# Performance work log

Measured on AMD Instinct MI355X. Metric: run time of the kernel, lower is better.

Reference implementation:

```python
import jax, jax.numpy as jnp
import numpy as np

B, S, D = 2, 2048, 768
E, L = 4, 2
H = 4 * D  # dim_mlp = dim * mlp_ratio
EPS = 1e-6


def setup_inputs() -> dict:
    key = jax.random.key(0)
    ks = jax.random.split(key, 4)
    x = jax.random.normal(ks[0], (B, S, D), dtype=jnp.float32)
    expert_idx = jax.random.randint(ks[1], (B, S), 0, E, dtype=jnp.int32)
    # Linear weights: normal(std=0.02), biases zero (per init_weights).
    W1 = 0.02 * jax.random.normal(ks[2], (L, E, D, H), dtype=jnp.float32)
    b1 = jnp.zeros((L, E, H), dtype=jnp.float32)
    W2 = 0.02 * jax.random.normal(ks[3], (L, E, H, D), dtype=jnp.float32)
    b2 = jnp.zeros((L, E, D), dtype=jnp.float32)
    # LayerNorm: weight=1, bias=0 (per init_weights).
    ln_g = jnp.ones((L, D), dtype=jnp.float32)
    ln_b = jnp.zeros((L, D), dtype=jnp.float32)
    return {"x": x, "expert_idx": expert_idx, "W1": W1, "b1": b1,
            "W2": W2, "b2": b2, "ln_g": ln_g, "ln_b": ln_b}


def _layernorm(x, g, b):
    mu = jnp.mean(x, axis=-1, keepdims=True)
    var = jnp.mean(jnp.square(x - mu), axis=-1, keepdims=True)
    return (x - mu) * jax.lax.rsqrt(var + EPS) * g + b


def reference(x, expert_idx, W1, b1, W2, b2, ln_g, ln_b):
    # Eval mode: Dropout and DropPath are identity.
    idx = expert_idx[:, :, None, None]  # [B,S,1,1] for gather over expert axis
    for i in range(L):
        h = _layernorm(x, ln_g[i], ln_b[i])                       # [B,S,D]
        # All experts' FFNs computed densely (as in the torch module).
        a = jnp.einsum('bsd,edh->bseh', h, W1[i]) + b1[i]         # [B,S,E,H]
        a = jax.nn.gelu(a, approximate=False)                     # exact GELU (nn.GELU)
        y = jnp.einsum('bseh,ehd->bsed', a, W2[i]) + b2[i]        # [B,S,E,D] == feat_all
        # Per-token gather of the selected expert's slice.
        sel = jnp.take_along_axis(y, idx, axis=2)[:, :, 0, :]     # [B,S,D]
        x = x + sel
    return x
```

## Files before the change

### kernel.cpp

```cpp
#include <hip/hip_runtime.h>
#include <hip/hip_bf16.h>

#define T_TOK 4096
#define DD 768
#define HH 3072
#define EE 4
#define LL 2
#define NELT (T_TOK * DD)

typedef __attribute__((ext_vector_type(8))) short short8;
typedef __attribute__((ext_vector_type(4))) float f32x4;

__device__ __forceinline__ float bf2f(ushort u) { return __uint_as_float(((unsigned)u) << 16); }
__device__ __forceinline__ ushort f2bf(float f) {
  unsigned x = __float_as_uint(f);
  return (ushort)((x + 0x7fffu + ((x >> 16) & 1u)) >> 16);
}

__device__ __forceinline__ void gl2lds16(const void* g, void* l) {
  __builtin_amdgcn_global_load_lds((const __attribute__((address_space(1))) void*)g,
                                   (__attribute__((address_space(3))) void*)l, 16, 0, 0);
}

__global__ __launch_bounds__(256) void prep_kernel(const int* __restrict__ eidx,
                                                   int* __restrict__ inv,
                                                   int* __restrict__ meta) {
  __shared__ int cnt[EE], cur[EE], offs[EE];
  int t = threadIdx.x;
  if (t < EE) { cnt[t] = 0; cur[t] = 0; }
  __syncthreads();
  for (int i = t; i < T_TOK; i += 256) atomicAdd(&cnt[eidx[i]], 1);
  __syncthreads();
  if (t == 0) {
    int off = 0, nt = 0;
    for (int e = 0; e < EE; e++) {
      meta[e] = off; offs[e] = off;
      int c = cnt[e];
      int n = (c + 127) >> 7;
      for (int k = 0; k < n; k++) { meta[8 + nt] = e; meta[96 + nt] = k << 7; nt++; }
      off += c;
    }
    meta[4] = off;
    meta[5] = nt;
  }
  __syncthreads();
  for (int i = t; i < T_TOK; i += 256) {
    int e = eidx[i];
    inv[i] = offs[e] + atomicAdd(&cur[e], 1);
  }
}

template <bool HASY, bool WRITEX>
__global__ __launch_bounds__(256) void ln_kernel(const float* __restrict__ x,
                                                 const float* __restrict__ y,
                                                 const float* __restrict__ g,
                                                 const float* __restrict__ b,
                                                 const int* __restrict__ inv,
                                                 ushort* __restrict__ h,
                                                 float* __restrict__ xf) {
  int wid = blockIdx.x * 4 + (threadIdx.x >> 6);
  int lane = threadIdx.x & 63;
  int pos = inv[wid];
  const float* xr = x + (size_t)wid * DD;
  const float* y0 = y + (size_t)pos * DD;
  const float* y1 = y0 + NELT;
  float v[12], s = 0.f, ss = 0.f;
#pragma unroll
  for (int i = 0; i < 12; i++) {
    int c = lane + i * 64;
    float vv = xr[c];
    if (HASY) vv += y0[c] + y1[c];
    if (WRITEX) xf[(size_t)wid * DD + c] = vv;
    v[i] = vv;
    s += vv; ss += vv * vv;
  }
#pragma unroll
  for (int o = 32; o; o >>= 1) { s += __shfl_xor(s, o, 64); ss += __shfl_xor(ss, o, 64); }
  float mu = s * (1.f / DD);
  float var = ss * (1.f / DD) - mu * mu;
  float rs = rsqrtf(var + 1e-6f);
  ushort* hr = h + (size_t)pos * DD;
#pragma unroll
  for (int i = 0; i < 12; i++) {
    int c = lane + i * 64;
    hr[c] = f2bf((v[i] - mu) * rs * g[c] + b[c]);
  }
}

__global__ __launch_bounds__(256) void store_kernel(const float* __restrict__ xf,
                                                    const float* __restrict__ y,
                                                    const int* __restrict__ inv,
                                                    float* __restrict__ out) {
  int wid = blockIdx.x * 4 + (threadIdx.x >> 6);
  int lane = threadIdx.x & 63;
  int pos = inv[wid];
  const float* xr = xf + (size_t)wid * DD;
  const float* y0 = y + (size_t)pos * DD;
  const float* y1 = y0 + NELT;
  float* o = out + (size_t)wid * DD;
#pragma unroll
  for (int i = 0; i < 12; i++) {
    int c = lane + i * 64;
    o[c] = xr[c] + y0[c] + y1[c];
  }
}

__global__ __launch_bounds__(256) void transpose_f32_bf16(const float* __restrict__ src,
                                                          ushort* __restrict__ dst,
                                                          int R, int C) {
  __shared__ ushort tile[64][68];
  size_t mo = (size_t)blockIdx.z * R * C;
  src += mo;
  dst += mo;
  int c0 = blockIdx.x * 64, r0 = blockIdx.y * 64;
  int t = threadIdx.x;
  int tr = t >> 4;
  int tc = (t & 15) << 2;
#pragma unroll
  for (int i = 0; i < 4; i++) {
    int r = tr + i * 16;
    float4 v = *(const float4*)(src + (size_t)(r0 + r) * C + (c0 + tc));
    tile[r][tc] = f2bf(v.x); tile[r][tc + 1] = f2bf(v.y);
    tile[r][tc + 2] = f2bf(v.z); tile[r][tc + 3] = f2bf(v.w);
  }
  __syncthreads();
#pragma unroll
  for (int i = 0; i < 4; i++) {
    int c = tr + i * 16;
    ushort4 v;
    v.x = tile[tc][c]; v.y = tile[tc + 1][c]; v.z = tile[tc + 2][c]; v.w = tile[tc + 3][c];
    *(ushort4*)(dst + (size_t)(c0 + c) * R + (r0 + tc)) = v;
  }
}

template <int KTOT, int KLEN, int NTOT, bool GELU>
__global__ __launch_bounds__(256, 2) void gemm_kernel(const ushort* __restrict__ A,
                                                      const ushort* __restrict__ Bt,
                                                      const float* __restrict__ bias,
                                                      void* __restrict__ Cout,
                                                      const int* __restrict__ meta) {
  int gx = gridDim.x;
  int nwg = gx * gridDim.y;
  int wgid = blockIdx.y * gx + blockIdx.x;
  int sq = nwg >> 3, sr = nwg & 7;
  int xcd = wgid & 7, sidx = wgid >> 3;
  int sw = (xcd < sr ? xcd * (sq + 1) : sr * (sq + 1) + (xcd - sr) * sq) + sidx;
  int ntile = sw % gx;
  int ty = sw / gx;

  if (ty >= meta[5]) return;
  int e = meta[8 + ty];
  int mstart = meta[96 + ty];
  int off0 = meta[e];
  int cnt = meta[e + 1] - off0;
  int z = blockIdx.z;
  int kbegin = z * KLEN;

  __shared__ __align__(16) ushort lds[32768];

  int tid = threadIdx.x;
  int w = tid >> 6, lane = tid & 63;

  int rr = lane >> 3;
  int swz = ((lane & 7) ^ rr) * 8;
  const ushort* agp[4];
  const ushort* bgp[4];
  int aoff[4];
  int boff[4];
#pragma unroll
  for (int i = 0; i < 4; i++) {
    int r = w * 32 + i * 8;
    int arow = off0 + min(mstart + r + rr, cnt - 1);
    agp[i] = A + (size_t)arow * KTOT + kbegin + swz;
    aoff[i] = r * 64 + lane * 8;
  }
#pragma unroll
  for (int i = 0; i < 4; i++) {
    int r = w * 32 + i * 8;
    int brow = e * NTOT + ntile * 128 + r + rr;
    bgp[i] = Bt + (size_t)brow * KTOT + kbegin + swz;
    boff[i] = 8192 + r * 64 + lane * 8;
  }

  int wm = (w >> 1) * 64, wn = (w & 1) * 64;
  int qm = lane & 15;
  int quad = lane >> 4;
  int s7 = qm & 7;

  f32x4 acc[4][4];
#pragma unroll
  for (int mi = 0; mi < 4; mi++)
#pragma unroll
    for (int ni = 0; ni < 4; ni++) acc[mi][ni] = (f32x4){0.f, 0.f, 0.f, 0.f};

#define STAGE(nb, koff)                                            \
  do {                                                             \
    ushort* _b = lds + (nb) * 16384;                               \
    _Pragma("unroll")                                              \
    for (int _i = 0; _i < 4; _i++) gl2lds16(agp[_i] + (koff), _b + aoff[_i]); \
    _Pragma("unroll")                                              \
    for (int _i = 0; _i < 4; _i++) gl2lds16(bgp[_i] + (koff), _b + boff[_i]); \
  } while (0)

  constexpr int NSTEPS = KLEN / 64;
  STAGE(0, 0);
  asm volatile("" ::: "memory");

#pragma unroll 1
  for (int s = 0; s < NSTEPS; ++s) {
    int curb = s & 1;
    if (s + 1 < NSTEPS) {
      STAGE(curb ^ 1, (s + 1) * 64);
      asm volatile("s_waitcnt vmcnt(8)" ::: "memory");
    } else {
      asm volatile("s_waitcnt vmcnt(0)" ::: "memory");
    }
    __builtin_amdgcn_s_barrier();
    asm volatile("" ::: "memory");

    const ushort* Asb = lds + curb * 16384;
    const ushort* Bsb = Asb + 8192;
#pragma unroll
    for (int h2 = 0; h2 < 2; h2++) {
      int lchunk = ((h2 * 4 + quad) ^ s7) * 8;
      short8 af[4], bfr[4];
#pragma unroll
      for (int mi = 0; mi < 4; mi++)
        af[mi] = *(const short8*)(Asb + (wm + mi * 16 + qm) * 64 + lchunk);
#pragma unroll
      for (int ni = 0; ni < 4; ni++)
        bfr[ni] = *(const short8*)(Bsb + (wn + ni * 16 + qm) * 64 + lchunk);
#pragma unroll
      for (int mi = 0; mi < 4; mi++)
#pragma unroll
        for (int ni = 0; ni < 4; ni++)
          acc[mi][ni] = __builtin_amdgcn_mfma_f32_16x16x32_bf16(af[mi], bfr[ni], acc[mi][ni], 0, 0, 0);
    }
    asm volatile("" ::: "memory");
    __builtin_amdgcn_s_barrier();
    asm volatile("" ::: "memory");
  }
#undef STAGE

  int rbase = quad * 4;
  float bv[4];
#pragma unroll
  for (int ni = 0; ni < 4; ni++)
    bv[ni] = (!GELU && z != 0) ? 0.f : bias[e * NTOT + ntile * 128 + wn + ni * 16 + qm];

  if (GELU) {
#pragma unroll
    for (int mi = 0; mi < 4; mi++)
#pragma unroll
      for (int ni = 0; ni < 4; ni++) {
        int c = wn + ni * 16 + qm;
#pragma unroll
        for (int r = 0; r < 4; r++) {
          float vv = acc[mi][ni][r] + bv[ni];
          vv = 0.5f * vv * (1.f + erff(vv * 0.70710678118f));
          lds[(wm + mi * 16 + rbase + r) * 128 + c] = f2bf(vv);
        }
      }
    __syncthreads();
    int row0 = tid >> 4;
    int cseg = (tid & 15) * 8;
    ushort* aout = (ushort*)Cout;
#pragma unroll
    for (int it = 0; it < 8; it++) {
      int row = it * 16 + row0;
      int mg = mstart + row;
      if (mg < cnt) {
        short8 v = *(const short8*)(lds + row * 128 + cseg);
        *(short8*)(aout + (size_t)(off0 + mg) * HH + ntile * 128 + cseg) = v;
      }
    }
  } else {
    float* y = (float*)Cout + (size_t)z * NELT;
#pragma unroll
    for (int mi = 0; mi < 4; mi++) {
#pragma unroll
      for (int r = 0; r < 4; r++) {
        int mg = mstart + wm + mi * 16 + rbase + r;
        if (mg >= cnt) continue;
        float* crow = y + (size_t)(off0 + mg) * DD + ntile * 128;
#pragma unroll
        for (int ni = 0; ni < 4; ni++)
          crow[wn + ni * 16 + qm] = acc[mi][ni][r] + bv[ni];
      }
    }
  }
}

extern "C" void kernel_launch(void* const* d_in, const int* in_sizes, int n_in,
                              void* d_out, int out_size, void* d_ws, size_t ws_size,
                              hipStream_t stream) {
  const float* x   = (const float*)d_in[0];
  const int*  eidx = (const int*)d_in[1];
  const float* W1  = (const float*)d_in[2];
  const float* b1  = (const float*)d_in[3];
  const float* W2  = (const float*)d_in[4];
  const float* b2  = (const float*)d_in[5];
  const float* lng = (const float*)d_in[6];
  const float* lnb = (const float*)d_in[7];

  char* ws = (char*)d_ws;
  float*  xf   = (float*)(ws + 0);
  ushort* h    = (ushort*)(ws + 12582912);
  ushort* a    = (ushort*)(ws + 18874368);
  ushort* Wt   = (ushort*)(ws + 44040192);
  float*  y    = (float*)(ws + 62914560);
  int*    inv  = (int*)(ws + 88080384);
  int*    meta = (int*)(ws + 88096768);

  prep_kernel<<<1, 256, 0, stream>>>(eidx, inv, meta);

  for (int l = 0; l < LL; l++) {
    if (l == 0)
      ln_kernel<false, false><<<T_TOK / 4, 256, 0, stream>>>(
          x, y, lng, lnb, inv, h, xf);
    else
      ln_kernel<true, true><<<T_TOK / 4, 256, 0, stream>>>(
          x, y, lng + l * DD, lnb + l * DD, inv, h, xf);
    transpose_f32_bf16<<<dim3(HH / 64, DD / 64, EE), 256, 0, stream>>>(
        W1 + (size_t)l * EE * DD * HH, Wt, DD, HH);
    gemm_kernel<DD, DD, HH, true><<<dim3(HH / 128, 35), 256, 0, stream>>>(
        h, Wt, b1 + l * EE * HH, (void*)a, meta);
    transpose_f32_bf16<<<dim3(DD / 64, HH / 64, EE), 256, 0, stream>>>(
        W2 + (size_t)l * EE * HH * DD, Wt, HH, DD);
    gemm_kernel<HH, HH / 2, DD, false><<<dim3(DD / 128, 35, 2), 256, 0, stream>>>(
        a, Wt, b2 + l * EE * DD, (void*)y, meta);
  }

  store_kernel<<<T_TOK / 4, 256, 0, stream>>>(xf, y, inv, (float*)d_out);
}
```

Measured before the change: 378.2 us.

## Replace double-buffered GEMM pipeline with single buffer and higher occupancy

Drops the double-buffered LDS prefetch pipeline in the expert GEMM kernel and uses a single 32KB LDS buffer. Each K step now loads, synchronizes, computes and synchronizes again. Launch bounds go from 2 to 4 blocks per CU, so latency hiding is meant to come from occupancy rather than explicit prefetch. The tighter register budget (128 VGPRs) with a 64-register accumulator plus fragments risks spills, and loads no longer overlap with MFMA work inside a block.

Result: slower. 460.4 us (+21.7%).

```diff
diff --git a/kernel.cpp b/kernel.cpp
--- a/kernel.cpp
+++ b/kernel.cpp
@@ -134,7 +134,7 @@
 }
 
 template <int KTOT, int KLEN, int NTOT, bool GELU>
-__global__ __launch_bounds__(256, 2) void gemm_kernel(const ushort* __restrict__ A,
+__global__ __launch_bounds__(256, 4) void gemm_kernel(const ushort* __restrict__ A,
                                                       const ushort* __restrict__ Bt,
                                                       const float* __restrict__ bias,
                                                       void* __restrict__ Cout,
@@ -156,7 +156,7 @@
   int z = blockIdx.z;
   int kbegin = z * KLEN;
 
-  __shared__ __align__(16) ushort lds[32768];
+  __shared__ __align__(16) ushort lds[16384];
 
   int tid = threadIdx.x;
   int w = tid >> 6, lane = tid & 63;
@@ -193,33 +193,15 @@
 #pragma unroll
     for (int ni = 0; ni < 4; ni++) acc[mi][ni] = (f32x4){0.f, 0.f, 0.f, 0.f};
 
-#define STAGE(nb, koff)                                            \
-  do {                                                             \
-    ushort* _b = lds + (nb) * 16384;                               \
-    _Pragma("unroll")                                              \
-    for (int _i = 0; _i < 4; _i++) gl2lds16(agp[_i] + (koff), _b + aoff[_i]); \
-    _Pragma("unroll")                                              \
-    for (int _i = 0; _i < 4; _i++) gl2lds16(bgp[_i] + (koff), _b + boff[_i]); \
-  } while (0)
-
-  constexpr int NSTEPS = KLEN / 64;
-  STAGE(0, 0);
-  asm volatile("" ::: "memory");
-
-#pragma unroll 1
-  for (int s = 0; s < NSTEPS; ++s) {
-    int curb = s & 1;
-    if (s + 1 < NSTEPS) {
-      STAGE(curb ^ 1, (s + 1) * 64);
-      asm volatile("s_waitcnt vmcnt(8)" ::: "memory");
-    } else {
-      asm volatile("s_waitcnt vmcnt(0)" ::: "memory");
-    }
-    __builtin_amdgcn_s_barrier();
-    asm volatile("" ::: "memory");
-
-    const ushort* Asb = lds + curb * 16384;
-    const ushort* Bsb = Asb + 8192;
+  for (int k0 = 0; k0 < KLEN; k0 += 64) {
+#pragma unroll
+    for (int i = 0; i < 4; i++) gl2lds16(agp[i] + k0, lds + aoff[i]);
+#pragma unroll
+    for (int i = 0; i < 4; i++) gl2lds16(bgp[i] + k0, lds + boff[i]);
+    __syncthreads();
+
+    const ushort* Asb = lds;
+    const ushort* Bsb = lds + 8192;
 #pragma unroll
     for (int h2 = 0; h2 < 2; h2++) {
       int lchunk = ((h2 * 4 + quad) ^ s7) * 8;
@@ -236,11 +218,8 @@
         for (int ni = 0; ni < 4; ni++)
           acc[mi][ni] = __builtin_amdgcn_mfma_f32_16x16x32_bf16(af[mi], bfr[ni], acc[mi][ni], 0, 0, 0);
     }
-    asm volatile("" ::: "memory");
-    __builtin_amdgcn_s_barrier();
-    asm volatile("" ::: "memory");
-  }
-#undef STAGE
+    __syncthreads();
+  }
 
   int rbase = quad * 4;
   float bv[4];
```

## Use 256x256 tiled GEMM with LDS-staged epilogue for first expert FFN layer

Applied to the files above, without the earlier changes.

Adds a new 512-thread GEMM kernel with 256x256 output tiles and matching 256-row expert tile metadata, and uses it for the first (D->H) grouped GEMM with fused bias and GELU. Larger tiles raise arithmetic intensity and cut redundant global loads of A and B. The epilogue stages bf16 results in LDS for coalesced 16-byte row stores. The cost is more padding waste for partially filled 256-row expert tiles, fewer workgroups (12x19), and heavy register and LDS use (128 KB LDS) that limits occupancy.

New measurement: 375.4 us. Within noise of the previous version (-0.8%).

```diff
diff --git a/kernel.cpp b/kernel.cpp
--- a/kernel.cpp
+++ b/kernel.cpp
@@ -32,16 +32,19 @@
   for (int i = t; i < T_TOK; i += 256) atomicAdd(&cnt[eidx[i]], 1);
   __syncthreads();
   if (t == 0) {
-    int off = 0, nt = 0;
+    int off = 0, nt = 0, nt2 = 0;
     for (int e = 0; e < EE; e++) {
       meta[e] = off; offs[e] = off;
       int c = cnt[e];
       int n = (c + 127) >> 7;
       for (int k = 0; k < n; k++) { meta[8 + nt] = e; meta[96 + nt] = k << 7; nt++; }
+      int n2 = (c + 255) >> 8;
+      for (int k = 0; k < n2; k++) { meta[160 + nt2] = e; meta[224 + nt2] = k << 8; nt2++; }
       off += c;
     }
     meta[4] = off;
     meta[5] = nt;
+    meta[6] = nt2;
   }
   __syncthreads();
   for (int i = t; i < T_TOK; i += 256) {
@@ -291,6 +294,140 @@
   }
 }
 
+template <int KTOT, int KLEN, int NTOT>
+__global__ __launch_bounds__(512, 2) void gemm256_kernel(const ushort* __restrict__ A,
+                                                         const ushort* __restrict__ Bt,
+                                                         const float* __restrict__ bias,
+                                                         ushort* __restrict__ aout,
+                                                         const int* __restrict__ meta) {
+  int gx = gridDim.x;
+  int nwg = gx * gridDim.y;
+  int wgid = blockIdx.y * gx + blockIdx.x;
+  int sq = nwg >> 3, sr = nwg & 7;
+  int xcd = wgid & 7, sidx = wgid >> 3;
+  int sw = (xcd < sr ? xcd * (sq + 1) : sr * (sq + 1) + (xcd - sr) * sq) + sidx;
+  int ntile = sw % gx;
+  int ty = sw / gx;
+
+  if (ty >= meta[6]) return;
+  int e = meta[160 + ty];
+  int mstart = meta[224 + ty];
+  int off0 = meta[e];
+  int cnt = meta[e + 1] - off0;
+
+  __shared__ __align__(16) ushort lds[65536];
+
+  int tid = threadIdx.x;
+  int w = tid >> 6, lane = tid & 63;
+
+  int rr = lane >> 3;
+  int swz = ((lane & 7) ^ rr) * 8;
+  const ushort* agp[4];
+  const ushort* bgp[4];
+  int aoff[4];
+  int boff[4];
+#pragma unroll
+  for (int i = 0; i < 4; i++) {
+    int r = w * 32 + i * 8;
+    int arow = off0 + min(mstart + r + rr, cnt - 1);
+    agp[i] = A + (size_t)arow * KTOT + swz;
+    aoff[i] = r * 64 + lane * 8;
+    int brow = e * NTOT + ntile * 256 + r + rr;
+    bgp[i] = Bt + (size_t)brow * KTOT + swz;
+    boff[i] = 16384 + r * 64 + lane * 8;
+  }
+
+  int wm = (w >> 2) * 128, wn = (w & 3) * 64;
+  int qm = lane & 15;
+  int quad = lane >> 4;
+  int s7 = qm & 7;
+
+  f32x4 acc[8][4];
+#pragma unroll
+  for (int mi = 0; mi < 8; mi++)
+#pragma unroll
+    for (int ni = 0; ni < 4; ni++) acc[mi][ni] = (f32x4){0.f, 0.f, 0.f, 0.f};
+
+#define STAGE2(nb, koff)                                           \
+  do {                                                             \
+    ushort* _b = lds + (nb) * 32768;                               \
+    _Pragma("unroll")                                              \
+    for (int _i = 0; _i < 4; _i++) gl2lds16(agp[_i] + (koff), _b + aoff[_i]); \
+    _Pragma("unroll")                                              \
+    for (int _i = 0; _i < 4; _i++) gl2lds16(bgp[_i] + (koff), _b + boff[_i]); \
+  } while (0)
+
+  constexpr int NSTEPS = KLEN / 64;
+  STAGE2(0, 0);
+  asm volatile("" ::: "memory");
+
+#pragma unroll 1
+  for (int s = 0; s < NSTEPS; ++s) {
+    int curb = s & 1;
+    if (s + 1 < NSTEPS) {
+      STAGE2(curb ^ 1, (s + 1) * 64);
+      asm volatile("s_waitcnt vmcnt(8)" ::: "memory");
+    } else {
+      asm volatile("s_waitcnt vmcnt(0)" ::: "memory");
+    }
+    __builtin_amdgcn_s_barrier();
+    asm volatile("" ::: "memory");
+
+    const ushort* Asb = lds + curb * 32768;
+    const ushort* Bsb = Asb + 16384;
+#pragma unroll
+    for (int h2 = 0; h2 < 2; h2++) {
+      int lchunk = ((h2 * 4 + quad) ^ s7) * 8;
+      short8 bfr[4];
+#pragma unroll
+      for (int ni = 0; ni < 4; ni++)
+        bfr[ni] = *(const short8*)(Bsb + (wn + ni * 16 + qm) * 64 + lchunk);
+#pragma unroll
+      for (int mi = 0; mi < 8; mi++) {
+        short8 af = *(const short8*)(Asb + (wm + mi * 16 + qm) * 64 + lchunk);
+#pragma unroll
+        for (int ni = 0; ni < 4; ni++)
+          acc[mi][ni] = __builtin_amdgcn_mfma_f32_16x16x32_bf16(af, bfr[ni], acc[mi][ni], 0, 0, 0);
+      }
+    }
+    asm volatile("" ::: "memory");
+    __builtin_amdgcn_s_barrier();
+    asm volatile("" ::: "memory");
+  }
+#undef STAGE2
+
+  int rbase = quad * 4;
+  float bv[4];
+#pragma unroll
+  for (int ni = 0; ni < 4; ni++)
+    bv[ni] = bias[e * NTOT + ntile * 256 + wn + ni * 16 + qm];
+
+#pragma unroll
+  for (int mi = 0; mi < 8; mi++)
+#pragma unroll
+    for (int ni = 0; ni < 4; ni++) {
+      int c = wn + ni * 16 + qm;
+#pragma unroll
+      for (int r = 0; r < 4; r++) {
+        float vv = acc[mi][ni][r] + bv[ni];
+        vv = 0.5f * vv * (1.f + erff(vv * 0.70710678118f));
+        lds[(wm + mi * 16 + rbase + r) * 256 + c] = f2bf(vv);
+      }
+    }
+  __syncthreads();
+  int row0 = tid >> 5;
+  int cseg = (tid & 31) * 8;
+#pragma unroll
+  for (int it = 0; it < 16; it++) {
+    int row = it * 16 + row0;
+    int mg = mstart + row;
+    if (mg < cnt) {
+      short8 v = *(const short8*)(lds + row * 256 + cseg);
+      *(short8*)(aout + (size_t)(off0 + mg) * HH + ntile * 256 + cseg) = v;
+    }
+  }
+}
+
 extern "C" void kernel_launch(void* const* d_in, const int* in_sizes, int n_in,
                               void* d_out, int out_size, void* d_ws, size_t ws_size,
                               hipStream_t stream) {
@@ -323,8 +460,8 @@
           x, y, lng + l * DD, lnb + l * DD, inv, h, xf);
     transpose_f32_bf16<<<dim3(HH / 64, DD / 64, EE), 256, 0, stream>>>(
         W1 + (size_t)l * EE * DD * HH, Wt, DD, HH);
-    gemm_kernel<DD, DD, HH, true><<<dim3(HH / 128, 35), 256, 0, stream>>>(
-        h, Wt, b1 + l * EE * HH, (void*)a, meta);
+    gemm256_kernel<DD, DD, HH><<<dim3(HH / 256, 19), 512, 0, stream>>>(
+        h, Wt, b1 + l * EE * HH, a, meta);
     transpose_f32_bf16<<<dim3(DD / 64, HH / 64, EE), 256, 0, stream>>>(
         W2 + (size_t)l * EE * HH * DD, Wt, HH, DD);
     gemm_kernel<HH, HH / 2, DD, false><<<dim3(DD / 128, 35, 2), 256, 0, stream>>>(
```
